# Performance work log

Hardware: AMD Instinct MI355X
Metric: run time of the kernel (lower is better)

## Reference

```python
import jax, jax.numpy as jnp
import numpy as np

KERNEL_SIZE = 4
SCALE_FACTOR = 0.5


def setup_inputs() -> dict:
    key = jax.random.key(0)
    k1, k2, k3 = jax.random.split(key, 3)
    batch, in_f, out_f = 4096, 2048, 4096
    x = jax.random.normal(k1, (batch, in_f), dtype=jnp.float32)
    # kaiming-uniform-like scale for weights
    W = jax.random.normal(k2, (out_f, in_f), dtype=jnp.float32) * (1.0 / np.sqrt(in_f))
    b = jax.random.normal(k3, (out_f,), dtype=jnp.float32) * (1.0 / np.sqrt(in_f))
    return {"x": x, "W": W, "b": b}


def reference(x, W, b):
    # Linear: (B, out_f)
    y = jnp.einsum("bi,oi->bo", x, W) + b
    B, out_f = y.shape
    groups = out_f // KERNEL_SIZE
    # MaxPool1d(kernel_size, stride=kernel_size) over feature dim
    pooled = jnp.max(y.reshape(B, groups, KERNEL_SIZE), axis=-1)  # (B, groups)
    # sum over pooled features, then scale -> (B,)
    return jnp.sum(pooled, axis=-1) * SCALE_FACTOR
```

## Files before the change

### kernel.cpp

```cpp
#include <hip/hip_runtime.h>


typedef float  f32x4   __attribute__((ext_vector_type(4)));
typedef short  bf16x8  __attribute__((ext_vector_type(8)));
typedef short  short4v __attribute__((ext_vector_type(4)));

__device__ __forceinline__ short f2bf(float f) {
    union { float f; unsigned u; } v; v.f = f;
    unsigned r = v.u + 0x7FFFu + ((v.u >> 16) & 1u);
    return (short)(r >> 16);
}

__global__ void cvt_kernel(const float* __restrict__ x, const float* __restrict__ w,
                           short* __restrict__ out, long nx, long nw,
                           float* __restrict__ zout, int zn) {
    long stride = (long)gridDim.x * blockDim.x;
    long tid0   = (long)blockIdx.x * blockDim.x + threadIdx.x;
    for (long i = tid0; i < zn; i += stride) zout[i] = 0.f;
    long total4 = (nx + nw) >> 2;
    for (long i = tid0; i < total4; i += stride) {
        long e = i << 2;
        const float* src = (e < nx) ? (x + e) : (w + (e - nx));
        float4 v = *(const float4*)src;
        short4v s = { f2bf(v.x), f2bf(v.y), f2bf(v.z), f2bf(v.w) };
        *(short4v*)(out + e) = s;
    }
}


#define GLL(gp, ldsp)                                                          \
    __builtin_amdgcn_global_load_lds(                                          \
        (const __attribute__((address_space(1))) unsigned int*)(gp),           \
        (__attribute__((address_space(3))) unsigned int*)(ldsp), 16, 0, 0)

__global__ __launch_bounds__(512, 1) void gemm_pool_kernel(
    const short* __restrict__ X, const short* __restrict__ W,
    const float* __restrict__ bias, float* __restrict__ out, int K)
{
    __shared__ short As[32768];
    __shared__ short Bs[32768];

    const int tid  = threadIdx.x;
    const int lane = tid & 63;
    const int wid  = tid >> 6;
    const int wr   = wid >> 2;
    const int wc   = wid & 3;
    const int hi   = lane >> 4;
    const int lo   = lane & 15;

    const int nwg  = gridDim.x * gridDim.y;
    const int bid  = blockIdx.y * gridDim.x + blockIdx.x;
    const int wgid = (bid & 7) * (nwg >> 3) + (bid >> 3);
    const int brow = (wgid / gridDim.x) * 256;
    const int bcol = (wgid % gridDim.x) * 256;
    const int nk   = K >> 6;

    const int slot0 = hi ^ (lo & 7);
    const int slot1 = (4 + hi) ^ (lo & 7);
    const char* baseA0 = (const char*)As + (((wr * 16 + (lo >> 3)) * 512 + (lo & 7) * 64 + slot0 * 8) << 1);
    const char* baseA1 = (const char*)As + (((wr * 16 + (lo >> 3)) * 512 + (lo & 7) * 64 + slot1 * 8) << 1);
    const char* baseB0 = (const char*)Bs + (((wc * 8  + (lo >> 3)) * 512 + (lo & 7) * 64 + slot0 * 8) << 1);
    const char* baseB1 = (const char*)Bs + (((wc * 8  + (lo >> 3)) * 512 + (lo & 7) * 64 + slot1 * 8) << 1);

    const int idx0 = wid * 2, idx1 = wid * 2 + 1;
    const int cA00 = (idx0 & 7) + ((idx0 >> 3) << 4), cA10 = (idx1 & 7) + ((idx1 >> 3) << 4);
    const int cA01 = cA00 + 8,                         cA11 = cA10 + 8;
    const int cB00 = ((idx0 >> 2) << 3) + (idx0 & 3),  cB10 = ((idx1 >> 2) << 3) + (idx1 & 3);
    const int cB01 = cB00 + 4,                         cB11 = cB10 + 4;
    const int grow = lane >> 3;
    const int gq8  = ((lane & 7) ^ (lane >> 3)) * 8;

    const short* pA00 = X + (size_t)(brow + cA00 * 8 + grow) * K + gq8;
    const short* pA10 = X + (size_t)(brow + cA10 * 8 + grow) * K + gq8;
    const short* pA01 = X + (size_t)(brow + cA01 * 8 + grow) * K + gq8;
    const short* pA11 = X + (size_t)(brow + cA11 * 8 + grow) * K + gq8;
    const short* pB00 = W + (size_t)(bcol + cB00 * 8 + grow) * K + gq8;
    const short* pB10 = W + (size_t)(bcol + cB10 * 8 + grow) * K + gq8;
    const short* pB01 = W + (size_t)(bcol + cB01 * 8 + grow) * K + gq8;
    const short* pB11 = W + (size_t)(bcol + cB11 * 8 + grow) * K + gq8;

    f32x4 acc[8][4] = {};
    bf16x8 a[4][2], b0[2][2], b1[2][2];

    GLL(pA00, As + cA00 * 512); GLL(pA10, As + cA10 * 512);
    GLL(pB00, Bs + cB00 * 512); GLL(pB10, Bs + cB10 * 512);
    GLL(pB01, Bs + cB01 * 512); GLL(pB11, Bs + cB11 * 512);
    GLL(pA01, As + cA01 * 512); GLL(pA11, As + cA11 * 512);
    GLL(pA00 + 64, As + 16384 + cA00 * 512); GLL(pA10 + 64, As + 16384 + cA10 * 512);
    GLL(pB01 + 64, Bs + 16384 + cB01 * 512); GLL(pB11 + 64, Bs + 16384 + cB11 * 512);
    GLL(pA01 + 64, As + 16384 + cA01 * 512); GLL(pA11 + 64, As + 16384 + cA11 * 512);
    pA00 += 128; pA10 += 128; pA01 += 128; pA11 += 128;
    pB00 += 128; pB10 += 128; pB01 += 128; pB11 += 128;
    asm volatile("s_waitcnt vmcnt(6)" ::: "memory");

#define TILE_BODY(T, BUF)                                                          \
    {                                                                              \
                  \
        __builtin_amdgcn_s_barrier();                                              \
        _Pragma("unroll")                                                          \
        for (int nn = 0; nn < 2; ++nn) {                                           \
            b0[nn][0] = *(const bf16x8*)(baseB0 + (BUF)*32768 + nn*2048);          \
            b0[nn][1] = *(const bf16x8*)(baseB1 + (BUF)*32768 + nn*2048);          \
        }                                                                          \
        _Pragma("unroll")                                                          \
        for (int mm = 0; mm < 4; ++mm) {                                           \
            a[mm][0] = *(const bf16x8*)(baseA0 + (BUF)*32768 + mm*2048);           \
            a[mm][1] = *(const bf16x8*)(baseA1 + (BUF)*32768 + mm*2048);           \
        }                                                                          \
        if ((T) + 1 < nk) {                                                        \
            GLL(pB00 - 64, Bs + (1-(BUF))*16384 + cB00*512);                       \
            GLL(pB10 - 64, Bs + (1-(BUF))*16384 + cB10*512);                       \
        }                                                                          \
        __builtin_amdgcn_s_setprio(1);                                             \
        _Pragma("unroll")                                                          \
        for (int mm = 0; mm < 4; ++mm)                                             \
            _Pragma("unroll")                                                      \
            for (int nn = 0; nn < 2; ++nn)                                         \
                _Pragma("unroll")                                                  \
                for (int kk = 0; kk < 2; ++kk)                                     \
                    acc[mm][nn] = __builtin_amdgcn_mfma_f32_16x16x32_bf16(         \
                        a[mm][kk], b0[nn][kk], acc[mm][nn], 0, 0, 0);              \
        __builtin_amdgcn_s_setprio(0);                                             \
                         \
        __builtin_amdgcn_s_barrier();                                              \
        _Pragma("unroll")                                                          \
        for (int nn = 0; nn < 2; ++nn) {                                           \
            b1[nn][0] = *(const bf16x8*)(baseB0 + (BUF)*32768 + nn*2048 + 4096);   \
            b1[nn][1] = *(const bf16x8*)(baseB1 + (BUF)*32768 + nn*2048 + 4096);   \
        }                                                                          \
        if ((T) + 2 < nk) {                                                        \
            GLL(pA00, As + (BUF)*16384 + cA00*512);                                \
            GLL(pA10, As + (BUF)*16384 + cA10*512);                                \
        }                                                                          \
        __builtin_amdgcn_s_setprio(1);                                             \
        _Pragma("unroll")                                                          \
        for (int mm = 0; mm < 4; ++mm)                                             \
            _Pragma("unroll")                                                      \
            for (int nn = 0; nn < 2; ++nn)                                         \
                _Pragma("unroll")                                                  \
                for (int kk = 0; kk < 2; ++kk)                                     \
                    acc[mm][2+nn] = __builtin_amdgcn_mfma_f32_16x16x32_bf16(       \
                        a[mm][kk], b1[nn][kk], acc[mm][2+nn], 0, 0, 0);            \
        __builtin_amdgcn_s_setprio(0);                                             \
                \
        __builtin_amdgcn_s_barrier();                                              \
        _Pragma("unroll")                                                          \
        for (int mm = 0; mm < 4; ++mm) {                                           \
            a[mm][0] = *(const bf16x8*)(baseA0 + (BUF)*32768 + mm*2048 + 8192);    \
            a[mm][1] = *(const bf16x8*)(baseA1 + (BUF)*32768 + mm*2048 + 8192);    \
        }                                                                          \
        if ((T) + 2 < nk) {                                                        \
            GLL(pB01, Bs + (BUF)*16384 + cB01*512);                                \
            GLL(pB11, Bs + (BUF)*16384 + cB11*512);                                \
        }                                                                          \
        __builtin_amdgcn_s_setprio(1);                                             \
        _Pragma("unroll")                                                          \
        for (int mm = 0; mm < 4; ++mm)                                             \
            _Pragma("unroll")                                                      \
            for (int nn = 0; nn < 2; ++nn)                                         \
                _Pragma("unroll")                                                  \
                for (int kk = 0; kk < 2; ++kk)                                     \
                    acc[4+mm][2+nn] = __builtin_amdgcn_mfma_f32_16x16x32_bf16(     \
                        a[mm][kk], b1[nn][kk], acc[4+mm][2+nn], 0, 0, 0);          \
        __builtin_amdgcn_s_setprio(0);                                             \
                  \
        __builtin_amdgcn_s_barrier();                                              \
        if ((T) + 2 < nk) {                                                        \
            GLL(pA01, As + (BUF)*16384 + cA01*512);                                \
            GLL(pA11, As + (BUF)*16384 + cA11*512);                                \
        }                                                                          \
        __builtin_amdgcn_s_setprio(1);                                             \
        _Pragma("unroll")                                                          \
        for (int mm = 0; mm < 4; ++mm)                                             \
            _Pragma("unroll")                                                      \
            for (int nn = 0; nn < 2; ++nn)                                         \
                _Pragma("unroll")                                                  \
                for (int kk = 0; kk < 2; ++kk)                                     \
                    acc[4+mm][nn] = __builtin_amdgcn_mfma_f32_16x16x32_bf16(       \
                        a[mm][kk], b0[nn][kk], acc[4+mm][nn], 0, 0, 0);            \
        __builtin_amdgcn_s_setprio(0);                                             \
        if ((T) == nk - 2)      asm volatile("s_waitcnt vmcnt(0)" ::: "memory");   \
        else if ((T) < nk - 2)  asm volatile("s_waitcnt vmcnt(6)" ::: "memory");   \
        pA00 += 64; pA10 += 64; pA01 += 64; pA11 += 64;                            \
        pB00 += 64; pB10 += 64; pB01 += 64; pB11 += 64;                            \
    }

    for (int t = 0; t < nk; t += 2) {
        TILE_BODY(t, 0);
        TILE_BODY(t + 1, 1);
    }
#undef TILE_BODY

    float bias_n[4];
#pragma unroll
    for (int nn = 0; nn < 4; ++nn)
        bias_n[nn] = bias[bcol + wc * 64 + nn * 16 + lo];

#pragma unroll
    for (int mm = 0; mm < 8; ++mm) {
#pragma unroll
        for (int j = 0; j < 4; ++j) {
            float part = 0.f;
#pragma unroll
            for (int nn = 0; nn < 4; ++nn) {
                float v = acc[mm][nn][j] + bias_n[nn];
                v = fmaxf(v, __shfl_xor(v, 1));
                v = fmaxf(v, __shfl_xor(v, 2));
                part += v;
            }
            part += __shfl_xor(part, 4);
            part += __shfl_xor(part, 8);
            if (lo == 0)
                atomicAdd(&out[brow + wr * 128 + mm * 16 + hi * 4 + j], part * 0.5f);
        }
    }
}

extern "C" void kernel_launch(void* const* d_in, const int* in_sizes, int n_in,
                              void* d_out, int out_size, void* d_ws, size_t ws_size,
                              hipStream_t stream) {
    const float* x = (const float*)d_in[0];
    const float* W = (const float*)d_in[1];
    const float* b = (const float*)d_in[2];
    float* out = (float*)d_out;

    const int N = in_sizes[2];
    const int K = in_sizes[1] / N;
    const int M = in_sizes[0] / K;

    short* xb = (short*)d_ws;
    short* wb = xb + in_sizes[0];
    cvt_kernel<<<2048, 256, 0, stream>>>(x, W, (short*)d_ws,
                                         (long)in_sizes[0], (long)in_sizes[1],
                                         out, out_size);

    dim3 grid(N / 256, M / 256);
    gemm_pool_kernel<<<grid, 512, 0, stream>>>(xb, wb, b, out, K);
}
```

Baseline: 85.32 us.

## Switch GEMM inner loop to 32x32x16 bf16 MFMA with rotated LDS swizzle

Replaces the 16x16x32 MFMA tiling with 32x32x16 MFMA tiles, which changes the per-wave accumulator layout (4x2 f32x16) and how fragments are loaded from LDS. It adds a new LDS swizzle with a per-chunk rotation, matched by rotated global source offsets, so the wider fragment reads avoid bank conflicts. The epilogue is rewritten for the 32x32 output layout with an extra shuffle level. The aim is fewer MFMA issues and fewer LDS reads per unit of work, at the cost of a more intricate index mapping that could break correctness if wrong.

```diff
diff --git a/kernel.cpp b/kernel.cpp
--- a/kernel.cpp
+++ b/kernel.cpp
@@ -1,7 +1,7 @@
 #include <hip/hip_runtime.h>
 
 
-typedef float  f32x4   __attribute__((ext_vector_type(4)));
+typedef float  f32x16  __attribute__((ext_vector_type(16)));
 typedef short  bf16x8  __attribute__((ext_vector_type(8)));
 typedef short  short4v __attribute__((ext_vector_type(4)));
 
@@ -27,7 +27,6 @@
     }
 }
 
-
 #define GLL(gp, ldsp)                                                          \
     __builtin_amdgcn_global_load_lds(                                          \
         (const __attribute__((address_space(1))) unsigned int*)(gp),           \
@@ -45,8 +44,8 @@
     const int wid  = tid >> 6;
     const int wr   = wid >> 2;
     const int wc   = wid & 3;
-    const int hi   = lane >> 4;
-    const int lo   = lane & 15;
+    const int lo32 = lane & 31;
+    const int hi32 = lane >> 5;
 
     const int nwg  = gridDim.x * gridDim.y;
     const int bid  = blockIdx.y * gridDim.x + blockIdx.x;
@@ -55,12 +54,21 @@
     const int bcol = (wgid % gridDim.x) * 256;
     const int nk   = K >> 6;
 
-    const int slot0 = hi ^ (lo & 7);
-    const int slot1 = (4 + hi) ^ (lo & 7);
-    const char* baseA0 = (const char*)As + (((wr * 16 + (lo >> 3)) * 512 + (lo & 7) * 64 + slot0 * 8) << 1);
-    const char* baseA1 = (const char*)As + (((wr * 16 + (lo >> 3)) * 512 + (lo & 7) * 64 + slot1 * 8) << 1);
-    const char* baseB0 = (const char*)Bs + (((wc * 8  + (lo >> 3)) * 512 + (lo & 7) * 64 + slot0 * 8) << 1);
-    const char* baseB1 = (const char*)Bs + (((wc * 8  + (lo >> 3)) * 512 + (lo & 7) * 64 + slot1 * 8) << 1);
+    int offA[4], offB[4];
+    {
+        const int rot = 2 * (((lane & 31) >> 3) & 3);
+        const int cbA = (wr * 16 + ((lane & 31) >> 3)) * 1024 + (lane & 7) * 128;
+        const int cbB = (wc * 8  + ((lane & 31) >> 3)) * 1024 + (lane & 7) * 128;
+#pragma unroll
+        for (int ks = 0; ks < 4; ++ks) {
+            const int q  = 2 * ks + hi32;
+            const int sg = (((q ^ (lane & 7)) + rot) & 7) * 16;
+            offA[ks] = cbA + sg;
+            offB[ks] = cbB + sg;
+        }
+    }
+    const char* Ab8 = (const char*)As;
+    const char* Bb8 = (const char*)Bs;
 
     const int idx0 = wid * 2, idx1 = wid * 2 + 1;
     const int cA00 = (idx0 & 7) + ((idx0 >> 3) << 4), cA10 = (idx1 & 7) + ((idx1 >> 3) << 4);
@@ -68,19 +76,20 @@
     const int cB00 = ((idx0 >> 2) << 3) + (idx0 & 3),  cB10 = ((idx1 >> 2) << 3) + (idx1 & 3);
     const int cB01 = cB00 + 4,                         cB11 = cB10 + 4;
     const int grow = lane >> 3;
-    const int gq8  = ((lane & 7) ^ (lane >> 3)) * 8;
-
-    const short* pA00 = X + (size_t)(brow + cA00 * 8 + grow) * K + gq8;
-    const short* pA10 = X + (size_t)(brow + cA10 * 8 + grow) * K + gq8;
-    const short* pA01 = X + (size_t)(brow + cA01 * 8 + grow) * K + gq8;
-    const short* pA11 = X + (size_t)(brow + cA11 * 8 + grow) * K + gq8;
-    const short* pB00 = W + (size_t)(bcol + cB00 * 8 + grow) * K + gq8;
-    const short* pB10 = W + (size_t)(bcol + cB10 * 8 + grow) * K + gq8;
-    const short* pB01 = W + (size_t)(bcol + cB01 * 8 + grow) * K + gq8;
-    const short* pB11 = W + (size_t)(bcol + cB11 * 8 + grow) * K + gq8;
-
-    f32x4 acc[8][4] = {};
-    bf16x8 a[4][2], b0[2][2], b1[2][2];
+#define QSRC(c) ((((((lane & 7) - 2 * ((c) & 3)) & 7) ^ (lane >> 3))) * 8)
+
+    const short* pA00 = X + (size_t)(brow + cA00 * 8 + grow) * K + QSRC(cA00);
+    const short* pA10 = X + (size_t)(brow + cA10 * 8 + grow) * K + QSRC(cA10);
+    const short* pA01 = X + (size_t)(brow + cA01 * 8 + grow) * K + QSRC(cA01);
+    const short* pA11 = X + (size_t)(brow + cA11 * 8 + grow) * K + QSRC(cA11);
+    const short* pB00 = W + (size_t)(bcol + cB00 * 8 + grow) * K + QSRC(cB00);
+    const short* pB10 = W + (size_t)(bcol + cB10 * 8 + grow) * K + QSRC(cB10);
+    const short* pB01 = W + (size_t)(bcol + cB01 * 8 + grow) * K + QSRC(cB01);
+    const short* pB11 = W + (size_t)(bcol + cB11 * 8 + grow) * K + QSRC(cB11);
+#undef QSRC
+
+    f32x16 acc[4][2] = {};
+    bf16x8 a[2][4], b0[4], b1[4];
 
     GLL(pA00, As + cA00 * 512); GLL(pA10, As + cA10 * 512);
     GLL(pB00, Bs + cB00 * 512); GLL(pB10, Bs + cB10 * 512);
@@ -95,75 +104,62 @@
 
 #define TILE_BODY(T, BUF)                                                          \
     {                                                                              \
-                  \
-        __builtin_amdgcn_s_barrier();                                              \
-        _Pragma("unroll")                                                          \
-        for (int nn = 0; nn < 2; ++nn) {                                           \
-            b0[nn][0] = *(const bf16x8*)(baseB0 + (BUF)*32768 + nn*2048);          \
-            b0[nn][1] = *(const bf16x8*)(baseB1 + (BUF)*32768 + nn*2048);          \
-        }                                                                          \
-        _Pragma("unroll")                                                          \
-        for (int mm = 0; mm < 4; ++mm) {                                           \
-            a[mm][0] = *(const bf16x8*)(baseA0 + (BUF)*32768 + mm*2048);           \
-            a[mm][1] = *(const bf16x8*)(baseA1 + (BUF)*32768 + mm*2048);           \
-        }                                                                          \
+          \
+        __builtin_amdgcn_s_barrier();                                              \
+        _Pragma("unroll")                                                          \
+        for (int ks = 0; ks < 4; ++ks)                                             \
+            b0[ks] = *(const bf16x8*)(Bb8 + (BUF)*32768 + offB[ks]);               \
+        _Pragma("unroll")                                                          \
+        for (int mq = 0; mq < 2; ++mq)                                             \
+            _Pragma("unroll")                                                      \
+            for (int ks = 0; ks < 4; ++ks)                                         \
+                a[mq][ks] = *(const bf16x8*)(Ab8 + (BUF)*32768 + offA[ks] + mq*4096); \
         if ((T) + 1 < nk) {                                                        \
             GLL(pB00 - 64, Bs + (1-(BUF))*16384 + cB00*512);                       \
             GLL(pB10 - 64, Bs + (1-(BUF))*16384 + cB10*512);                       \
         }                                                                          \
         __builtin_amdgcn_s_setprio(1);                                             \
         _Pragma("unroll")                                                          \
-        for (int mm = 0; mm < 4; ++mm)                                             \
-            _Pragma("unroll")                                                      \
-            for (int nn = 0; nn < 2; ++nn)                                         \
-                _Pragma("unroll")                                                  \
-                for (int kk = 0; kk < 2; ++kk)                                     \
-                    acc[mm][nn] = __builtin_amdgcn_mfma_f32_16x16x32_bf16(         \
-                        a[mm][kk], b0[nn][kk], acc[mm][nn], 0, 0, 0);              \
-        __builtin_amdgcn_s_setprio(0);                                             \
-                         \
-        __builtin_amdgcn_s_barrier();                                              \
-        _Pragma("unroll")                                                          \
-        for (int nn = 0; nn < 2; ++nn) {                                           \
-            b1[nn][0] = *(const bf16x8*)(baseB0 + (BUF)*32768 + nn*2048 + 4096);   \
-            b1[nn][1] = *(const bf16x8*)(baseB1 + (BUF)*32768 + nn*2048 + 4096);   \
-        }                                                                          \
+        for (int ks = 0; ks < 4; ++ks) {                                           \
+            acc[0][0] = __builtin_amdgcn_mfma_f32_32x32x16_bf16(a[0][ks], b0[ks], acc[0][0], 0, 0, 0); \
+            acc[1][0] = __builtin_amdgcn_mfma_f32_32x32x16_bf16(a[1][ks], b0[ks], acc[1][0], 0, 0, 0); \
+        }                                                                          \
+        __builtin_amdgcn_s_setprio(0);                                             \
+                      \
+        __builtin_amdgcn_s_barrier();                                              \
+        _Pragma("unroll")                                                          \
+        for (int ks = 0; ks < 4; ++ks)                                             \
+            b1[ks] = *(const bf16x8*)(Bb8 + (BUF)*32768 + offB[ks] + 4096);        \
         if ((T) + 2 < nk) {                                                        \
             GLL(pA00, As + (BUF)*16384 + cA00*512);                                \
             GLL(pA10, As + (BUF)*16384 + cA10*512);                                \
         }                                                                          \
         __builtin_amdgcn_s_setprio(1);                                             \
         _Pragma("unroll")                                                          \
-        for (int mm = 0; mm < 4; ++mm)                                             \
+        for (int ks = 0; ks < 4; ++ks) {                                           \
+            acc[0][1] = __builtin_amdgcn_mfma_f32_32x32x16_bf16(a[0][ks], b1[ks], acc[0][1], 0, 0, 0); \
+            acc[1][1] = __builtin_amdgcn_mfma_f32_32x32x16_bf16(a[1][ks], b1[ks], acc[1][1], 0, 0, 0); \
+        }                                                                          \
+        __builtin_amdgcn_s_setprio(0);                                             \
+                  \
+        __builtin_amdgcn_s_barrier();                                              \
+        _Pragma("unroll")                                                          \
+        for (int mq = 0; mq < 2; ++mq)                                             \
             _Pragma("unroll")                                                      \
-            for (int nn = 0; nn < 2; ++nn)                                         \
-                _Pragma("unroll")                                                  \
-                for (int kk = 0; kk < 2; ++kk)                                     \
-                    acc[mm][2+nn] = __builtin_amdgcn_mfma_f32_16x16x32_bf16(       \
-                        a[mm][kk], b1[nn][kk], acc[mm][2+nn], 0, 0, 0);            \
-        __builtin_amdgcn_s_setprio(0);                                             \
-                \
-        __builtin_amdgcn_s_barrier();                                              \
-        _Pragma("unroll")                                                          \
-        for (int mm = 0; mm < 4; ++mm) {                                           \
-            a[mm][0] = *(const bf16x8*)(baseA0 + (BUF)*32768 + mm*2048 + 8192);    \
-            a[mm][1] = *(const bf16x8*)(baseA1 + (BUF)*32768 + mm*2048 + 8192);    \
-        }                                                                          \
+            for (int ks = 0; ks < 4; ++ks)                                         \
+                a[mq][ks] = *(const bf16x8*)(Ab8 + (BUF)*32768 + offA[ks] + 8192 + mq*4096); \
         if ((T) + 2 < nk) {                                                        \
             GLL(pB01, Bs + (BUF)*16384 + cB01*512);                                \
             GLL(pB11, Bs + (BUF)*16384 + cB11*512);                                \
         }                                                                          \
         __builtin_amdgcn_s_setprio(1);                                             \
         _Pragma("unroll")                                                          \
-        for (int mm = 0; mm < 4; ++mm)                                             \
-            _Pragma("unroll")                                                      \
-            for (int nn = 0; nn < 2; ++nn)                                         \
-                _Pragma("unroll")                                                  \
-                for (int kk = 0; kk < 2; ++kk)                                     \
-                    acc[4+mm][2+nn] = __builtin_amdgcn_mfma_f32_16x16x32_bf16(     \
-                        a[mm][kk], b1[nn][kk], acc[4+mm][2+nn], 0, 0, 0);          \
-        __builtin_amdgcn_s_setprio(0);                                             \
-                  \
+        for (int ks = 0; ks < 4; ++ks) {                                           \
+            acc[2][1] = __builtin_amdgcn_mfma_f32_32x32x16_bf16(a[0][ks], b1[ks], acc[2][1], 0, 0, 0); \
+            acc[3][1] = __builtin_amdgcn_mfma_f32_32x32x16_bf16(a[1][ks], b1[ks], acc[3][1], 0, 0, 0); \
+        }                                                                          \
+        __builtin_amdgcn_s_setprio(0);                                             \
+               \
         __builtin_amdgcn_s_barrier();                                              \
         if ((T) + 2 < nk) {                                                        \
             GLL(pA01, As + (BUF)*16384 + cA01*512);                                \
@@ -171,13 +167,10 @@
         }                                                                          \
         __builtin_amdgcn_s_setprio(1);                                             \
         _Pragma("unroll")                                                          \
-        for (int mm = 0; mm < 4; ++mm)                                             \
-            _Pragma("unroll")                                                      \
-            for (int nn = 0; nn < 2; ++nn)                                         \
-                _Pragma("unroll")                                                  \
-                for (int kk = 0; kk < 2; ++kk)                                     \
-                    acc[4+mm][nn] = __builtin_amdgcn_mfma_f32_16x16x32_bf16(       \
-                        a[mm][kk], b0[nn][kk], acc[4+mm][nn], 0, 0, 0);            \
+        for (int ks = 0; ks < 4; ++ks) {                                           \
+            acc[2][0] = __builtin_amdgcn_mfma_f32_32x32x16_bf16(a[0][ks], b0[ks], acc[2][0], 0, 0, 0); \
+            acc[3][0] = __builtin_amdgcn_mfma_f32_32x32x16_bf16(a[1][ks], b0[ks], acc[3][0], 0, 0, 0); \
+        }                                                                          \
         __builtin_amdgcn_s_setprio(0);                                             \
         if ((T) == nk - 2)      asm volatile("s_waitcnt vmcnt(0)" ::: "memory");   \
         else if ((T) < nk - 2)  asm volatile("s_waitcnt vmcnt(6)" ::: "memory");   \
@@ -191,27 +184,29 @@
     }
 #undef TILE_BODY
 
-    float bias_n[4];
-#pragma unroll
-    for (int nn = 0; nn < 4; ++nn)
-        bias_n[nn] = bias[bcol + wc * 64 + nn * 16 + lo];
-
-#pragma unroll
-    for (int mm = 0; mm < 8; ++mm) {
-#pragma unroll
-        for (int j = 0; j < 4; ++j) {
+    float bias_n[2];
+#pragma unroll
+    for (int nn = 0; nn < 2; ++nn)
+        bias_n[nn] = bias[bcol + wc * 64 + nn * 32 + lo32];
+
+#pragma unroll
+    for (int mq = 0; mq < 4; ++mq) {
+#pragma unroll
+        for (int r = 0; r < 16; ++r) {
             float part = 0.f;
 #pragma unroll
-            for (int nn = 0; nn < 4; ++nn) {
-                float v = acc[mm][nn][j] + bias_n[nn];
+            for (int nn = 0; nn < 2; ++nn) {
+                float v = acc[mq][nn][r] + bias_n[nn];
                 v = fmaxf(v, __shfl_xor(v, 1));
                 v = fmaxf(v, __shfl_xor(v, 2));
                 part += v;
             }
             part += __shfl_xor(part, 4);
             part += __shfl_xor(part, 8);
-            if (lo == 0)
-                atomicAdd(&out[brow + wr * 128 + mm * 16 + hi * 4 + j], part * 0.5f);
+            part += __shfl_xor(part, 16);
+            if (lo32 == 0)
+                atomicAdd(&out[brow + wr * 128 + mq * 32 +
+                               (r & 3) + 8 * (r >> 2) + 4 * hi32], part * 0.5f);
         }
     }
 }
```

Measured after the change: 124.7 us. +46.2%, slower.
